# Performance work log

Hardware: AMD Instinct MI355X
Metric: run time of the kernel (lower is better)

The kernel has to match this reference:

```python
import jax, jax.numpy as jnp
import numpy as np

EMBED_DIM = 768
N_HEADS = 12
HEAD_DIM = EMBED_DIM // N_HEADS
SCALE = HEAD_DIM ** 0.5


def setup_inputs() -> dict:
    key = jax.random.key(0)
    k1, k2, k3 = jax.random.split(key, 3)
    x = jax.random.normal(k1, (2, 2048, EMBED_DIM), dtype=jnp.float32)
    # weights stored [in, out] so forward is x @ W (equivalent to torch Linear with W.T)
    w_qkv = jax.random.normal(k2, (EMBED_DIM, 3 * EMBED_DIM), dtype=jnp.float32) * (EMBED_DIM ** -0.5)
    w_proj = jax.random.normal(k3, (EMBED_DIM, EMBED_DIM), dtype=jnp.float32) * (EMBED_DIM ** -0.5)
    return {"x": x, "w_qkv": w_qkv, "w_proj": w_proj}


def reference(x, w_qkv, w_proj):
    B, N, C = x.shape
    qkv = x @ w_qkv  # [B, N, 3C]
    qkv = qkv.reshape(B, N, 3, N_HEADS, HEAD_DIM)
    qkv = jnp.transpose(qkv, (2, 0, 3, 1, 4))  # [3, B, H, N, hd]
    q, k, v = qkv[0], qkv[1], qkv[2]
    attn = jnp.einsum("bhnd,bhmd->bhnm", q, k) / SCALE  # [B, H, N, N]
    attn = jax.nn.softmax(attn, axis=-1)
    out = jnp.einsum("bhnm,bhmd->bhnd", attn, v)  # [B, H, N, hd]
    out = jnp.transpose(out, (0, 2, 1, 3)).reshape(B, N, C)
    return out @ w_proj
```

## Files before the change

kernel.cpp:

```cpp
#include <hip/hip_runtime.h>
#include <hip/hip_bf16.h>
#include <stdint.h>

typedef uint16_t u16;
typedef __attribute__((ext_vector_type(4))) float f32x4;
typedef __attribute__((ext_vector_type(8))) short bf16x8;

#define LOG2E 1.4426950408889634f

static __device__ __forceinline__ u16 f2b(float x){
  union { float f; uint32_t u; } a; a.f = x;
  uint32_t r = a.u + 0x7FFFu + ((a.u >> 16) & 1u);
  return (u16)(r >> 16);
}

static __device__ __forceinline__ uint32_t pkrhu(float lo, float hi){
  union { float f; uint32_t u; } a, b; a.f = lo; b.f = hi;
  return __builtin_amdgcn_perm(b.u + 0x8000u, a.u + 0x8000u, 0x07060302u);
}

#define GLD16(g, l) __builtin_amdgcn_global_load_lds((const __attribute__((address_space(1))) void*)(g), (__attribute__((address_space(3))) void*)(l), 16, 0, 0)

__global__ __launch_bounds__(256) void k_cast(const float* __restrict__ in, u16* __restrict__ out, int n8){
  int i = blockIdx.x * 256 + threadIdx.x;
  if (i >= n8) return;
  const f32x4* p = (const f32x4*)(in + (size_t)i * 8);
  f32x4 a = p[0], b = p[1];
  u16 h[8];
#pragma unroll
  for (int j = 0; j < 4; ++j){ h[j] = f2b(a[j]); h[4+j] = f2b(b[j]); }
  *(bf16x8*)(out + (size_t)i * 8) = *(const bf16x8*)h;
}

__global__ void k_tcast(const float* __restrict__ in, u16* __restrict__ out, int R, int C){
  __shared__ float t[32][33];
  int c0 = blockIdx.x * 32, r0 = blockIdx.y * 32;
  int tx = threadIdx.x, ty = threadIdx.y;
#pragma unroll
  for (int i = 0; i < 32; i += 8) t[ty + i][tx] = in[(size_t)(r0 + ty + i) * C + c0 + tx];
  __syncthreads();
#pragma unroll
  for (int i = 0; i < 32; i += 8) out[(size_t)(c0 + ty + i) * R + r0 + tx] = f2b(t[tx][ty + i]);
}

__global__ __launch_bounds__(256) void k_gemmqkv(const u16* __restrict__ A, const u16* __restrict__ Bt,
                                                 u16* __restrict__ Qp, u16* __restrict__ Kp, u16* __restrict__ Vtp){
  __shared__ __align__(16) u16 SM[14336];
  u16* Al = SM; u16* Bl = SM + 8192;
  const int tid = threadIdx.x;
  const int w = tid >> 6, l = tid & 63;
  const int m0 = blockIdx.x * 128, n0 = blockIdx.y * 96;
  const int wm = (w >> 1) * 64, wn = (w & 1) * 48;
  const int lg = l >> 4, lr = l & 15;
  f32x4 acc[4][3] = {};
  const u16* asrc = A  + (size_t)(m0 + w*32 + (l >> 3)) * 768 + (l & 7) * 8;
  const u16* bsrc = Bt + (size_t)(n0 + w*24 + (l >> 3)) * 768 + (l & 7) * 8;
  for (int k0 = 0; k0 < 768; k0 += 64){
#pragma unroll
    for (int i = 0; i < 4; ++i)
      GLD16(asrc + (size_t)(i*8)*768 + k0, &Al[(w*32 + i*8) * 64]);
#pragma unroll
    for (int i = 0; i < 3; ++i)
      GLD16(bsrc + (size_t)(i*8)*768 + k0, &Bl[(w*24 + i*8) * 64]);
    __syncthreads();
    bf16x8 af[4][2], bfr[3][2];
#pragma unroll
    for (int mf = 0; mf < 4; ++mf)
#pragma unroll
      for (int ks = 0; ks < 2; ++ks)
        af[mf][ks] = *(const bf16x8*)&Al[(wm + mf*16 + lr) * 64 + ks*32 + lg*8];
#pragma unroll
    for (int nf = 0; nf < 3; ++nf)
#pragma unroll
      for (int ks = 0; ks < 2; ++ks)
        bfr[nf][ks] = *(const bf16x8*)&Bl[(wn + nf*16 + lr) * 64 + ks*32 + lg*8];
#pragma unroll
    for (int ks = 0; ks < 2; ++ks)
#pragma unroll
      for (int mf = 0; mf < 4; ++mf)
#pragma unroll
        for (int nf = 0; nf < 3; ++nf)
          acc[mf][nf] = __builtin_amdgcn_mfma_f32_16x16x32_bf16(af[mf][ks], bfr[nf][ks], acc[mf][nf], 0, 0, 0);
    __syncthreads();
  }

  const int which = n0 / 768;
  const int nl0 = n0 - which * 768;
  if (which < 2){
    u16* dst = (which == 0) ? Qp : Kp;
    const float sc = (which == 0) ? 0.125f * LOG2E : 1.0f;
#pragma unroll
    for (int mf = 0; mf < 4; ++mf)
#pragma unroll
      for (int nf = 0; nf < 3; ++nf)
#pragma unroll
        for (int r = 0; r < 4; ++r){
          int m = m0 + wm + mf*16 + lg*4 + r;
          int n = nl0 + wn + nf*16 + lr;
          int b = m >> 11, row = m & 2047, hh = n >> 6, d = n & 63;
          dst[(size_t)((b*12 + hh)*2048 + row) * 64 + d] = f2b(acc[mf][nf][r] * sc);
        }
  } else {
#pragma unroll
    for (int mf = 0; mf < 4; ++mf)
#pragma unroll
      for (int nf = 0; nf < 3; ++nf)
#pragma unroll
        for (int r = 0; r < 4; ++r){
          int mrow = wm + mf*16 + lg*4 + r;
          int c    = wn + nf*16 + lr;
          SM[c * 128 + mrow] = f2b(acc[mf][nf][r]);
        }
    __syncthreads();
#pragma unroll
    for (int rr = 0; rr < 6; ++rr){
      int c  = rr*16 + (tid >> 4);
      int mo = (tid & 15) * 8;
      bf16x8 v = *(const bf16x8*)&SM[c * 128 + mo];
      int n = nl0 + c, hh = n >> 6, d = n & 63;
      int m = m0 + mo, b = m >> 11, key = m & 2047;
      *(bf16x8*)&Vtp[(size_t)((b*12 + hh)*64 + d) * 2048 + key] = v;
    }
  }
}

__global__ __launch_bounds__(256) void k_gemm64(const u16* __restrict__ A, const u16* __restrict__ Bt,
                                                float* __restrict__ Co){
  __shared__ __align__(16) u16 SM[8192];
  u16* Al = SM; u16* Bl = SM + 4096;
  const int tid = threadIdx.x;
  const int w = tid >> 6, l = tid & 63;
  const int m0 = blockIdx.x * 64, n0 = blockIdx.y * 64;
  const int wm = (w >> 1) * 32, wn = (w & 1) * 32;
  const int lg = l >> 4, lr = l & 15;
  f32x4 acc[2][2] = {};
  const u16* asrc = A  + (size_t)(m0 + w*16 + (l >> 3)) * 768 + (l & 7) * 8;
  const u16* bsrc = Bt + (size_t)(n0 + w*16 + (l >> 3)) * 768 + (l & 7) * 8;
  for (int k0 = 0; k0 < 768; k0 += 64){
#pragma unroll
    for (int i = 0; i < 2; ++i){
      GLD16(asrc + (size_t)(i*8)*768 + k0, &Al[(w*16 + i*8) * 64]);
      GLD16(bsrc + (size_t)(i*8)*768 + k0, &Bl[(w*16 + i*8) * 64]);
    }
    __syncthreads();
    bf16x8 af[2][2], bfr[2][2];
#pragma unroll
    for (int mf = 0; mf < 2; ++mf)
#pragma unroll
      for (int ks = 0; ks < 2; ++ks){
        af[mf][ks]  = *(const bf16x8*)&Al[(wm + mf*16 + lr) * 64 + ks*32 + lg*8];
        bfr[mf][ks] = *(const bf16x8*)&Bl[(wn + mf*16 + lr) * 64 + ks*32 + lg*8];
      }
#pragma unroll
    for (int ks = 0; ks < 2; ++ks)
#pragma unroll
      for (int mf = 0; mf < 2; ++mf)
#pragma unroll
        for (int nf = 0; nf < 2; ++nf)
          acc[mf][nf] = __builtin_amdgcn_mfma_f32_16x16x32_bf16(af[mf][ks], bfr[nf][ks], acc[mf][nf], 0, 0, 0);
    __syncthreads();
  }
#pragma unroll
  for (int mf = 0; mf < 2; ++mf)
#pragma unroll
    for (int nf = 0; nf < 2; ++nf)
#pragma unroll
      for (int r = 0; r < 4; ++r)
        Co[(size_t)(m0 + wm + mf*16 + lg*4 + r) * 768 + n0 + wn + nf*16 + lr] = acc[mf][nf][r];
}

__global__ __launch_bounds__(256) void k_attn(const u16* __restrict__ Qp, const u16* __restrict__ Kp,
                                              const u16* __restrict__ Vtp, u16* __restrict__ AO){
  __shared__ __align__(16) u16 SM[16384];
  u16* Kl = SM; u16* Vl = SM + 8192;
  const int tid = threadIdx.x, w = tid >> 6, l = tid & 63;
  const int qh = w >> 1, kh = w & 1;
  const int lg = l >> 4, lr = l & 15;
  const int qt_b = blockIdx.x, bh = blockIdx.y;
  const int b = bh / 12, hh = bh - b * 12;
  const size_t base = (size_t)bh * (2048 * 64);
  const u16* Qg = Qp + base; const u16* Kg = Kp + base; const u16* Vg = Vtp + base;
  const int q0w = qt_b * 64 + qh * 32;
  const int rsw = (lr & 7) * 8;

  bf16x8 qf[2][2];
#pragma unroll
  for (int qt = 0; qt < 2; ++qt)
#pragma unroll
    for (int ks = 0; ks < 2; ++ks)
      qf[qt][ks] = *(const bf16x8*)&Qg[(size_t)(q0w + qt*16 + lr) * 64 + ks*32 + lg*8];

  f32x4 oacc[2][4] = {};
  float lp[2] = {0.f, 0.f};

  const int pl0 = w*8 + (l >> 3);
  const int sk0 = 8*((pl0 >> 2) & 3) + 4*((pl0 >> 4) & 1) + (pl0 & 3);
  const int csw = (((l & 7) ^ ((l >> 3) & 7)) << 3);
  const u16* kLp = Kg + (size_t)sk0 * 64 + csw;
  const u16* kUp = kLp + 32 * 64;
  const u16* vLp = Vg + ((size_t)pl0 << 11) + csw;
  const u16* vUp = vLp + ((size_t)32 << 11);
  u16* const K0lo = &Kl[0*4096 + (w*8)*64];
  u16* const K0hi = &Kl[0*4096 + (w*8+32)*64];
  u16* const K1lo = &Kl[1*4096 + (w*8)*64];
  u16* const K1hi = &Kl[1*4096 + (w*8+32)*64];
  u16* const V0lo = &Vl[0*4096 + (w*8)*64];
  u16* const V0hi = &Vl[0*4096 + (w*8+32)*64];
  u16* const V1lo = &Vl[1*4096 + (w*8)*64];
  u16* const V1hi = &Vl[1*4096 + (w*8+32)*64];

  auto compute = [&](const u16* Kc, const u16* Vc){
    f32x4 s[2][2] = {};
    bf16x8 kfr[2][2];
#pragma unroll
    for (int kf = 0; kf < 2; ++kf)
#pragma unroll
      for (int ks = 0; ks < 2; ++ks)
        kfr[kf][ks] = *(const bf16x8*)&Kc[(kh*32 + kf*16 + lr) * 64 + ((ks*32 + lg*8) ^ rsw)];
    __builtin_amdgcn_s_setprio(1);
#pragma unroll
    for (int ks = 0; ks < 2; ++ks)
#pragma unroll
      for (int kf = 0; kf < 2; ++kf)
#pragma unroll
        for (int qt = 0; qt < 2; ++qt)
          s[qt][kf] = __builtin_amdgcn_mfma_f32_16x16x32_bf16(kfr[kf][ks], qf[qt][ks], s[qt][kf], 0, 0, 0);
    __builtin_amdgcn_s_setprio(0);

    bf16x8 pa[2];
#pragma unroll
    for (int qt = 0; qt < 2; ++qt){
      float p00 = __builtin_exp2f(s[qt][0][0]);
      float p01 = __builtin_exp2f(s[qt][0][1]);
      float p02 = __builtin_exp2f(s[qt][0][2]);
      float p03 = __builtin_exp2f(s[qt][0][3]);
      float p10 = __builtin_exp2f(s[qt][1][0]);
      float p11 = __builtin_exp2f(s[qt][1][1]);
      float p12 = __builtin_exp2f(s[qt][1][2]);
      float p13 = __builtin_exp2f(s[qt][1][3]);
      lp[qt] += ((p00 + p01) + (p02 + p03)) + ((p10 + p11) + (p12 + p13));
      union { uint32_t u[4]; bf16x8 v; } fr;
      fr.u[0] = pkrhu(p00, p01);
      fr.u[1] = pkrhu(p02, p03);
      fr.u[2] = pkrhu(p10, p11);
      fr.u[3] = pkrhu(p12, p13);
      pa[qt] = fr.v;
    }

    bf16x8 vfr[4];
#pragma unroll
    for (int nf = 0; nf < 4; ++nf)
      vfr[nf] = *(const bf16x8*)&Vc[(nf*16 + lr) * 64 + ((kh*32 + lg*8) ^ rsw)];
    __builtin_amdgcn_s_setprio(1);
#pragma unroll
    for (int qt = 0; qt < 2; ++qt)
#pragma unroll
      for (int nf = 0; nf < 4; ++nf)
        oacc[qt][nf] = __builtin_amdgcn_mfma_f32_16x16x32_bf16(vfr[nf], pa[qt], oacc[qt][nf], 0, 0, 0);
    __builtin_amdgcn_s_setprio(0);
  };

  GLD16(kLp, K0lo); GLD16(kUp, K0hi); GLD16(vLp, V0lo); GLD16(vUp, V0hi);
  kLp += 4096; kUp += 4096; vLp += 64; vUp += 64;
  __syncthreads();

  for (int it = 0; it < 16; ++it){
    GLD16(kLp, K1lo); GLD16(kUp, K1hi); GLD16(vLp, V1lo); GLD16(vUp, V1hi);
    kLp += 4096; kUp += 4096; vLp += 64; vUp += 64;
    compute(&Kl[0], &Vl[0]);
    __syncthreads();
    if (it < 15){
      GLD16(kLp, K0lo); GLD16(kUp, K0hi); GLD16(vLp, V0lo); GLD16(vUp, V0hi);
      kLp += 4096; kUp += 4096; vLp += 64; vUp += 64;
    }
    compute(&Kl[4096], &Vl[4096]);
    __syncthreads();
  }

  float lt[2];
#pragma unroll
  for (int qt = 0; qt < 2; ++qt){
    float t = lp[qt];
    t += __shfl_xor(t, 16);
    t += __shfl_xor(t, 32);
    lt[qt] = t;
  }

  float* Osc = (float*)SM;
  float* Lsc = Osc + 64 * 65;
  if (kh == 1){
#pragma unroll
    for (int qt = 0; qt < 2; ++qt)
#pragma unroll
      for (int nf = 0; nf < 4; ++nf)
#pragma unroll
        for (int r = 0; r < 4; ++r)
          Osc[(qh*32 + qt*16 + lr) * 65 + nf*16 + lg*4 + r] = oacc[qt][nf][r];
    if (lg == 0){
      Lsc[qh*32 + lr]      = lt[0];
      Lsc[qh*32 + 16 + lr] = lt[1];
    }
  }
  __syncthreads();
  if (kh == 0){
#pragma unroll
    for (int qt = 0; qt < 2; ++qt){
      float inv = 1.0f / (lt[qt] + Lsc[qh*32 + qt*16 + lr]);
#pragma unroll
      for (int nf = 0; nf < 4; ++nf)
#pragma unroll
        for (int r = 0; r < 4; ++r){
          float o = oacc[qt][nf][r] + Osc[(qh*32 + qt*16 + lr) * 65 + nf*16 + lg*4 + r];
          AO[(size_t)((b << 11) + q0w + qt*16 + lr) * 768 + hh*64 + nf*16 + lg*4 + r] = f2b(o * inv);
        }
    }
  }
}

extern "C" void kernel_launch(void* const* d_in, const int* in_sizes, int n_in,
                              void* d_out, int out_size, void* d_ws, size_t ws_size,
                              hipStream_t stream){
  const float* x      = (const float*)d_in[0];
  const float* w_qkv  = (const float*)d_in[1];
  const float* w_proj = (const float*)d_in[2];
  float* out = (float*)d_out;
  char* ws = (char*)d_ws;
  u16* Xb     = (u16*)(ws + 0);
  u16* WqkvT  = (u16*)(ws + 6291456);
  u16* WprojT = (u16*)(ws + 9830400);
  u16* Qp     = (u16*)(ws + 11010048);
  u16* Kp     = (u16*)(ws + 17301504);
  u16* Vtp    = (u16*)(ws + 23592960);
  u16* AO     = (u16*)(ws + 29884416);

  k_cast<<<1536, 256, 0, stream>>>(x, Xb, 393216);
  k_tcast<<<dim3(72, 24), dim3(32, 8), 0, stream>>>(w_qkv, WqkvT, 768, 2304);
  k_tcast<<<dim3(24, 24), dim3(32, 8), 0, stream>>>(w_proj, WprojT, 768, 768);
  k_gemmqkv<<<dim3(32, 24), 256, 0, stream>>>(Xb, WqkvT, Qp, Kp, Vtp);
  k_attn<<<dim3(32, 24), 256, 0, stream>>>(Qp, Kp, Vtp, AO);
  k_gemm64<<<dim3(64, 12), 256, 0, stream>>>(AO, WprojT, out);
}
```

Before: 98.22 us.

## Triple-buffer attention K/V loads and merge cast kernels into one launch

The attention kernel moves from a double-buffered K/V pipeline with full __syncthreads to a three-stage ring buffer in 48KB of LDS. Explicit vmcnt(8) waits let two tiles stay in flight while the current one is computed. Separately, the x cast and the two weight transpose-casts are merged into one k_prep launch, removing two kernel launches. The larger LDS footprint may lower attention occupancy, and the hand-written waitcnt/barrier ordering is fragile.

```diff
diff --git a/kernel.cpp b/kernel.cpp
--- a/kernel.cpp
+++ b/kernel.cpp
@@ -21,21 +21,29 @@
 
 #define GLD16(g, l) __builtin_amdgcn_global_load_lds((const __attribute__((address_space(1))) void*)(g), (__attribute__((address_space(3))) void*)(l), 16, 0, 0)
 
-__global__ __launch_bounds__(256) void k_cast(const float* __restrict__ in, u16* __restrict__ out, int n8){
-  int i = blockIdx.x * 256 + threadIdx.x;
-  if (i >= n8) return;
-  const f32x4* p = (const f32x4*)(in + (size_t)i * 8);
-  f32x4 a = p[0], b = p[1];
-  u16 h[8];
-#pragma unroll
-  for (int j = 0; j < 4; ++j){ h[j] = f2b(a[j]); h[4+j] = f2b(b[j]); }
-  *(bf16x8*)(out + (size_t)i * 8) = *(const bf16x8*)h;
-}
-
-__global__ void k_tcast(const float* __restrict__ in, u16* __restrict__ out, int R, int C){
+__global__ __launch_bounds__(256) void k_prep(const float* __restrict__ x, u16* __restrict__ Xb,
+                                              const float* __restrict__ wqkv, u16* __restrict__ WqkvT,
+                                              const float* __restrict__ wproj, u16* __restrict__ WprojT){
   __shared__ float t[32][33];
-  int c0 = blockIdx.x * 32, r0 = blockIdx.y * 32;
-  int tx = threadIdx.x, ty = threadIdx.y;
+  const int bid = blockIdx.x, tid = threadIdx.x;
+  if (bid < 1536){
+    int i = bid * 256 + tid;
+    const f32x4* p = (const f32x4*)(x + (size_t)i * 8);
+    f32x4 a = p[0], b = p[1];
+    u16 h[8];
+#pragma unroll
+    for (int j = 0; j < 4; ++j){ h[j] = f2b(a[j]); h[4+j] = f2b(b[j]); }
+    *(bf16x8*)(Xb + (size_t)i * 8) = *(const bf16x8*)h;
+    return;
+  }
+  const float* in; u16* out; int R, C, bx, by;
+  if (bid < 1536 + 1728){
+    int q = bid - 1536; in = wqkv; out = WqkvT; R = 768; C = 2304; bx = q % 72; by = q / 72;
+  } else {
+    int q = bid - 1536 - 1728; in = wproj; out = WprojT; R = 768; C = 768; bx = q % 24; by = q / 24;
+  }
+  int c0 = bx * 32, r0 = by * 32;
+  int tx = tid & 31, ty = tid >> 5;
 #pragma unroll
   for (int i = 0; i < 32; i += 8) t[ty + i][tx] = in[(size_t)(r0 + ty + i) * C + c0 + tx];
   __syncthreads();
@@ -171,8 +179,7 @@
 
 __global__ __launch_bounds__(256) void k_attn(const u16* __restrict__ Qp, const u16* __restrict__ Kp,
                                               const u16* __restrict__ Vtp, u16* __restrict__ AO){
-  __shared__ __align__(16) u16 SM[16384];
-  u16* Kl = SM; u16* Vl = SM + 8192;
+  __shared__ __align__(16) u16 SM[24576];
   const int tid = threadIdx.x, w = tid >> 6, l = tid & 63;
   const int qh = w >> 1, kh = w & 1;
   const int lg = l >> 4, lr = l & 15;
@@ -200,14 +207,13 @@
   const u16* kUp = kLp + 32 * 64;
   const u16* vLp = Vg + ((size_t)pl0 << 11) + csw;
   const u16* vUp = vLp + ((size_t)32 << 11);
-  u16* const K0lo = &Kl[0*4096 + (w*8)*64];
-  u16* const K0hi = &Kl[0*4096 + (w*8+32)*64];
-  u16* const K1lo = &Kl[1*4096 + (w*8)*64];
-  u16* const K1hi = &Kl[1*4096 + (w*8+32)*64];
-  u16* const V0lo = &Vl[0*4096 + (w*8)*64];
-  u16* const V0hi = &Vl[0*4096 + (w*8+32)*64];
-  u16* const V1lo = &Vl[1*4096 + (w*8)*64];
-  u16* const V1hi = &Vl[1*4096 + (w*8+32)*64];
+  const int dlo = (w*8) * 64, dhi = (w*8 + 32) * 64;
+  u16* const K0lo = SM + 0     + dlo;  u16* const K0hi = SM + 0     + dhi;
+  u16* const K1lo = SM + 4096  + dlo;  u16* const K1hi = SM + 4096  + dhi;
+  u16* const K2lo = SM + 8192  + dlo;  u16* const K2hi = SM + 8192  + dhi;
+  u16* const V0lo = SM + 12288 + dlo;  u16* const V0hi = SM + 12288 + dhi;
+  u16* const V1lo = SM + 16384 + dlo;  u16* const V1hi = SM + 16384 + dhi;
+  u16* const V2lo = SM + 20480 + dlo;  u16* const V2hi = SM + 20480 + dhi;
 
   auto compute = [&](const u16* Kc, const u16* Vc){
     f32x4 s[2][2] = {};
@@ -260,22 +266,35 @@
     __builtin_amdgcn_s_setprio(0);
   };
 
-  GLD16(kLp, K0lo); GLD16(kUp, K0hi); GLD16(vLp, V0lo); GLD16(vUp, V0hi);
-  kLp += 4096; kUp += 4096; vLp += 64; vUp += 64;
-  __syncthreads();
-
-  for (int it = 0; it < 16; ++it){
-    GLD16(kLp, K1lo); GLD16(kUp, K1hi); GLD16(vLp, V1lo); GLD16(vUp, V1hi);
-    kLp += 4096; kUp += 4096; vLp += 64; vUp += 64;
-    compute(&Kl[0], &Vl[0]);
-    __syncthreads();
-    if (it < 15){
-      GLD16(kLp, K0lo); GLD16(kUp, K0hi); GLD16(vLp, V0lo); GLD16(vUp, V0hi);
-      kLp += 4096; kUp += 4096; vLp += 64; vUp += 64;
-    }
-    compute(&Kl[4096], &Vl[4096]);
-    __syncthreads();
-  }
+#define STAGE4(KL, KH, VL, VH) do { GLD16(kLp, KL); GLD16(kUp, KH); GLD16(vLp, VL); GLD16(vUp, VH); \
+                                    kLp += 4096; kUp += 4096; vLp += 64; vUp += 64; } while(0)
+#define BAR_CNT8  do { asm volatile("s_waitcnt vmcnt(8)" ::: "memory"); \
+                       __builtin_amdgcn_s_barrier(); __builtin_amdgcn_sched_barrier(0); } while(0)
+#define BAR_CNT0  do { asm volatile("s_waitcnt vmcnt(0)" ::: "memory"); \
+                       __builtin_amdgcn_s_barrier(); __builtin_amdgcn_sched_barrier(0); } while(0)
+
+  STAGE4(K0lo, K0hi, V0lo, V0hi);
+  STAGE4(K1lo, K1hi, V1lo, V1hi);
+  BAR_CNT8;
+
+  for (int g = 0; g < 10; ++g){
+    STAGE4(K2lo, K2hi, V2lo, V2hi);
+    compute(SM + 0,     SM + 12288);
+    BAR_CNT8;
+    STAGE4(K0lo, K0hi, V0lo, V0hi);
+    compute(SM + 4096,  SM + 16384);
+    BAR_CNT8;
+    STAGE4(K1lo, K1hi, V1lo, V1hi);
+    compute(SM + 8192,  SM + 20480);
+    BAR_CNT8;
+  }
+  compute(SM + 0,    SM + 12288);
+  BAR_CNT0;
+  compute(SM + 4096, SM + 16384);
+
+#undef STAGE4
+#undef BAR_CNT8
+#undef BAR_CNT0
 
   float lt[2];
 #pragma unroll
@@ -286,6 +305,7 @@
     lt[qt] = t;
   }
 
+  __syncthreads();
   float* Osc = (float*)SM;
   float* Lsc = Osc + 64 * 65;
   if (kh == 1){
@@ -333,9 +353,7 @@
   u16* Vtp    = (u16*)(ws + 23592960);
   u16* AO     = (u16*)(ws + 29884416);
 
-  k_cast<<<1536, 256, 0, stream>>>(x, Xb, 393216);
-  k_tcast<<<dim3(72, 24), dim3(32, 8), 0, stream>>>(w_qkv, WqkvT, 768, 2304);
-  k_tcast<<<dim3(24, 24), dim3(32, 8), 0, stream>>>(w_proj, WprojT, 768, 768);
+  k_prep<<<3840, 256, 0, stream>>>(x, Xb, w_qkv, WqkvT, w_proj, WprojT);
   k_gemmqkv<<<dim3(32, 24), 256, 0, stream>>>(Xb, WqkvT, Qp, Kp, Vtp);
   k_attn<<<dim3(32, 24), 256, 0, stream>>>(Qp, Kp, Vtp, AO);
   k_gemm64<<<dim3(64, 12), 256, 0, stream>>>(AO, WprojT, out);
```

New measurement: 91.41 us. 6.9% less time.
